# Kernel tuning notes

Measured on AMD Instinct MI355X. Metric: run time of the kernel, lower is better.

Reference implementation:

```python
import jax, jax.numpy as jnp
import numpy as np

N_NODES = 100000
F_IN, HID, OUT = 128, 64, 32


def setup_inputs() -> dict:
    key = jax.random.key(0)
    ks = jax.random.split(key, 16)
    x = jax.random.normal(ks[0], (N_NODES, F_IN), dtype=jnp.float32)
    edge_index = jax.random.randint(ks[1], (2, 3200000), 0, N_NODES, dtype=jnp.int64)
    edge_label_index = jax.random.randint(ks[2], (2, 1000000), 0, N_NODES, dtype=jnp.int64)
    def glorot(k, shape):
        lim = float(np.sqrt(6.0 / (shape[0] + shape[1])))
        return jax.random.uniform(k, shape, jnp.float32, -lim, lim)
    W1 = glorot(ks[3], (F_IN, HID)); b1 = jnp.zeros((HID,), jnp.float32)
    W2 = glorot(ks[4], (HID, HID)); b2 = jnp.zeros((HID,), jnp.float32)
    W3 = glorot(ks[5], (HID, OUT)); b3 = jnp.zeros((OUT,), jnp.float32)
    lpW1 = glorot(ks[6], (2 * OUT, HID)); lpb1 = jnp.zeros((HID,), jnp.float32)
    lpW2 = glorot(ks[7], (HID, 1)); lpb2 = jnp.zeros((1,), jnp.float32)
    return dict(x=x, edge_index=edge_index, edge_label_index=edge_label_index,
                W1=W1, b1=b1, W2=W2, b2=b2, W3=W3, b3=b3,
                lpW1=lpW1, lpb1=lpb1, lpW2=lpW2, lpb2=lpb2)


def _gcn_norm(edge_index, num_nodes):
    # PyG GCNConv default: add self-loops, symmetric normalization.
    self_loops = jnp.arange(num_nodes, dtype=edge_index.dtype)
    row = jnp.concatenate([edge_index[0], self_loops])  # source nodes
    col = jnp.concatenate([edge_index[1], self_loops])  # target nodes
    deg = jax.ops.segment_sum(jnp.ones_like(col, dtype=jnp.float32), col,
                              num_segments=num_nodes)
    dinv = jnp.where(deg > 0, jax.lax.rsqrt(deg), 0.0)
    norm = dinv[row] * dinv[col]  # [E + N]
    return row, col, norm


def _gcn_layer(x, W, b, row, col, norm, num_nodes):
    h = x @ W                               # [N, out]
    msg = h[row] * norm[:, None]            # gather + scale per edge
    agg = jax.ops.segment_sum(msg, col, num_segments=num_nodes)
    return agg + b


def reference(x, edge_index, edge_label_index, W1, b1, W2, b2, W3, b3,
              lpW1, lpb1, lpW2, lpb2):
    n = x.shape[0]
    row, col, norm = _gcn_norm(edge_index, n)
    # encode (eval mode: dropout is identity)
    z = jax.nn.relu(_gcn_layer(x, W1, b1, row, col, norm, n))
    z = jax.nn.relu(_gcn_layer(z, W2, b2, row, col, norm, n))
    z = _gcn_layer(z, W3, b3, row, col, norm, n)
    # decode: gather endpoint embeddings + MLP link predictor
    ef = jnp.concatenate([z[edge_label_index[0]], z[edge_label_index[1]]], axis=1)
    h = jax.nn.relu(ef @ lpW1 + lpb1)
    link_pred = h @ lpW2 + lpb2             # [E_label, 1]
    return link_pred, z
```

## Files before the change

### kernel.cpp

```cpp
#include <hip/hip_runtime.h>
#include <hip/hip_bf16.h>
#include <hip/hip_fp16.h>


#define BINA_CHUNK 8192


__global__ __launch_bounds__(512) void bhist_kernel(const int* __restrict__ colv,
                                                    int* __restrict__ chist,
                                                    int E, int nbuk) {
    __shared__ int hist[800];
    int base = blockIdx.x * BINA_CHUNK;
    int end = min(base + BINA_CHUNK, E);
    for (int i = threadIdx.x; i < nbuk; i += 512) hist[i] = 0;
    __syncthreads();
    int e = base + threadIdx.x * 4;
    for (; e + 4 <= end; e += 2048) {
        int4 c4 = *(const int4*)&colv[e];
        atomicAdd(&hist[c4.x >> 7], 1);
        atomicAdd(&hist[c4.y >> 7], 1);
        atomicAdd(&hist[c4.z >> 7], 1);
        atomicAdd(&hist[c4.w >> 7], 1);
    }
    for (; e < end; ++e) atomicAdd(&hist[colv[e] >> 7], 1);
    __syncthreads();
    for (int b = threadIdx.x; b < nbuk; b += 512)
        chist[(size_t)blockIdx.x * nbuk + b] = hist[b];
}


__global__ __launch_bounds__(256) void colscan_kernel(int* __restrict__ chist,
                                                      int* __restrict__ bcount,
                                                      int nchunk, int nbuk) {
    __shared__ int sh[256];
    const int b = blockIdx.x;
    const int c0 = threadIdx.x * 4;
    int v[4]; int s = 0;
#pragma unroll
    for (int i = 0; i < 4; ++i) {
        int c = c0 + i;
        v[i] = (c < nchunk) ? chist[(size_t)c * nbuk + b] : 0;
        s += v[i];
    }
    sh[threadIdx.x] = s;
    __syncthreads();
#pragma unroll
    for (int off = 1; off < 256; off <<= 1) {
        int y = (threadIdx.x >= (unsigned)off) ? sh[threadIdx.x - off] : 0;
        __syncthreads();
        sh[threadIdx.x] += y;
        __syncthreads();
    }
    int ex = sh[threadIdx.x] - s;
#pragma unroll
    for (int i = 0; i < 4; ++i) {
        int c = c0 + i;
        if (c < nchunk) { chist[(size_t)c * nbuk + b] = ex; ex += v[i]; }
    }
    if (threadIdx.x == 255) bcount[b] = sh[255];
}


__global__ __launch_bounds__(256) void bscan_kernel(const int* __restrict__ bcount,
                                                    int* __restrict__ bbase,
                                                    int nbuk, int* __restrict__ offsets, int N) {
    __shared__ int sh[256];
    int base = threadIdx.x * 4;
    int v[4]; int tsum = 0;
#pragma unroll
    for (int i = 0; i < 4; ++i) { int idx = base + i; v[i] = (idx < nbuk) ? bcount[idx] : 0; tsum += v[i]; }
    sh[threadIdx.x] = tsum;
    __syncthreads();
#pragma unroll
    for (int off = 1; off < 256; off <<= 1) {
        int y = (threadIdx.x >= (unsigned)off) ? sh[threadIdx.x - off] : 0;
        __syncthreads();
        sh[threadIdx.x] += y;
        __syncthreads();
    }
    int ex = sh[threadIdx.x] - tsum;
#pragma unroll
    for (int i = 0; i < 4; ++i) {
        int idx = base + i;
        if (idx < nbuk) { bbase[idx] = ex; ex += v[i]; }
        else if (idx == nbuk) { bbase[idx] = ex; offsets[N] = ex; }
    }
}


__global__ __launch_bounds__(512) void binA_kernel(const int* __restrict__ rowv,
                                                   const int* __restrict__ colv,
                                                   const int* __restrict__ chist,
                                                   const int* __restrict__ bbase,
                                                   int* __restrict__ pairs,
                                                   int E, int nbuk) {
    __shared__ int pos[800];
    int base = blockIdx.x * BINA_CHUNK;
    int end = min(base + BINA_CHUNK, E);
    for (int b = threadIdx.x; b < nbuk; b += 512)
        pos[b] = bbase[b] + chist[(size_t)blockIdx.x * nbuk + b];
    __syncthreads();
    int e = base + threadIdx.x * 4;
    for (; e + 4 <= end; e += 2048) {
        int4 c4 = *(const int4*)&colv[e];
        int4 r4 = *(const int4*)&rowv[e];
        int g0 = atomicAdd(&pos[c4.x >> 7], 1); pairs[g0] = (r4.x << 7) | (c4.x & 127);
        int g1 = atomicAdd(&pos[c4.y >> 7], 1); pairs[g1] = (r4.y << 7) | (c4.y & 127);
        int g2 = atomicAdd(&pos[c4.z >> 7], 1); pairs[g2] = (r4.z << 7) | (c4.z & 127);
        int g3 = atomicAdd(&pos[c4.w >> 7], 1); pairs[g3] = (r4.w << 7) | (c4.w & 127);
    }
    for (; e < end; ++e) {
        int c = colv[e];
        int g = atomicAdd(&pos[c >> 7], 1);
        pairs[g] = (rowv[e] << 7) | (c & 127);
    }
}


__global__ __launch_bounds__(512) void binB_kernel(const int* __restrict__ pairs,
                                                   const int* __restrict__ bbase,
                                                   int* __restrict__ offsets,
                                                   float* __restrict__ dinv,
                                                   int* __restrict__ edge_src, int N) {
    __shared__ int lcnt[128];
    __shared__ int sc[128];
    __shared__ int lcur[128];
    int nodeBeg = blockIdx.x << 7;
    int segBeg = bbase[blockIdx.x];
    int segEnd = bbase[blockIdx.x + 1];
    if (threadIdx.x < 128) lcnt[threadIdx.x] = 0;
    __syncthreads();
    for (int e = segBeg + threadIdx.x; e < segEnd; e += 512)
        atomicAdd(&lcnt[pairs[e] & 127], 1);
    __syncthreads();
    int v = (threadIdx.x < 128) ? lcnt[threadIdx.x] : 0;
    if (threadIdx.x < 128) sc[threadIdx.x] = v;
    __syncthreads();
    for (int off = 1; off < 128; off <<= 1) {
        int y = 0;
        if (threadIdx.x < 128 && threadIdx.x >= (unsigned)off) y = sc[threadIdx.x - off];
        __syncthreads();
        if (threadIdx.x < 128) sc[threadIdx.x] += y;
        __syncthreads();
    }
    if (threadIdx.x < 128) {
        int ex = sc[threadIdx.x] - v;
        lcur[threadIdx.x] = ex;
        int node = nodeBeg + threadIdx.x;
        if (node < N) {
            offsets[node] = segBeg + ex;
            dinv[node] = rsqrtf((float)(v + 1));
        }
    }
    __syncthreads();
    for (int e = segBeg + threadIdx.x; e < segEnd; e += 512) {
        int p = pairs[e];
        int rel = atomicAdd(&lcur[p & 127], 1);
        edge_src[segBeg + rel] = p >> 7;
    }
}


template <int K, int NOUT>
__global__ __launch_bounds__(32 * (NOUT / 4)) void gemm_scale(const float* __restrict__ in_,
                                                              const float* __restrict__ W,
                                                              const float* __restrict__ dinv,
                                                              __half* __restrict__ out, int N) {
    constexpr int TPB = 32 * (NOUT / 4);
    constexpr int KS = (K > 64) ? 64 : K;
    constexpr int XPITCH = KS + 4;
    __shared__ float xs[64 * XPITCH];
    __shared__ float ws[KS * NOUT];

    const int tid = threadIdx.x;
    const int nodeBase = blockIdx.x * 64;

    const int jg = tid % (NOUT / 4);
    const int ng = tid / (NOUT / 4);

    float acc[2][4];
#pragma unroll
    for (int i = 0; i < 2; ++i)
#pragma unroll
        for (int j = 0; j < 4; ++j) acc[i][j] = 0.f;

    for (int kh = 0; kh < K / KS; ++kh) {
        if (kh) __syncthreads();
        for (int i = tid; i < KS * NOUT / 4; i += TPB)
            *(float4*)&ws[i * 4] = *(const float4*)&W[(size_t)kh * KS * NOUT + i * 4];
        for (int i = tid; i < 64 * KS / 4; i += TPB) {
            int row = i / (KS / 4), c = i % (KS / 4);
            int src = nodeBase + row; if (src >= N) src = N - 1;
            *(float4*)&xs[row * XPITCH + c * 4] =
                *(const float4*)&in_[(size_t)src * K + kh * KS + c * 4];
        }
        __syncthreads();

#pragma unroll 4
        for (int kc = 0; kc < KS / 4; ++kc) {
            float4 xv[2], wv[4];
#pragma unroll
            for (int ni = 0; ni < 2; ++ni)
                xv[ni] = *(const float4*)&xs[(ng * 2 + ni) * XPITCH + kc * 4];
#pragma unroll
            for (int t = 0; t < 4; ++t)
                wv[t] = *(const float4*)&ws[(kc * 4 + t) * NOUT + jg * 4];
#pragma unroll
            for (int ni = 0; ni < 2; ++ni) {
                acc[ni][0] = fmaf(xv[ni].x, wv[0].x, acc[ni][0]);
                acc[ni][1] = fmaf(xv[ni].x, wv[0].y, acc[ni][1]);
                acc[ni][2] = fmaf(xv[ni].x, wv[0].z, acc[ni][2]);
                acc[ni][3] = fmaf(xv[ni].x, wv[0].w, acc[ni][3]);
                acc[ni][0] = fmaf(xv[ni].y, wv[1].x, acc[ni][0]);
                acc[ni][1] = fmaf(xv[ni].y, wv[1].y, acc[ni][1]);
                acc[ni][2] = fmaf(xv[ni].y, wv[1].z, acc[ni][2]);
                acc[ni][3] = fmaf(xv[ni].y, wv[1].w, acc[ni][3]);
                acc[ni][0] = fmaf(xv[ni].z, wv[2].x, acc[ni][0]);
                acc[ni][1] = fmaf(xv[ni].z, wv[2].y, acc[ni][1]);
                acc[ni][2] = fmaf(xv[ni].z, wv[2].z, acc[ni][2]);
                acc[ni][3] = fmaf(xv[ni].z, wv[2].w, acc[ni][3]);
                acc[ni][0] = fmaf(xv[ni].w, wv[3].x, acc[ni][0]);
                acc[ni][1] = fmaf(xv[ni].w, wv[3].y, acc[ni][1]);
                acc[ni][2] = fmaf(xv[ni].w, wv[3].z, acc[ni][2]);
                acc[ni][3] = fmaf(xv[ni].w, wv[3].w, acc[ni][3]);
            }
        }
    }

#pragma unroll
    for (int ni = 0; ni < 2; ++ni) {
        int node = nodeBase + ng * 2 + ni;
        if (node < N) {
            float dn = dinv[node];
            __half2* op = (__half2*)(out + (size_t)node * NOUT + jg * 4);
            op[0] = __floats2half2_rn(acc[ni][0] * dn, acc[ni][1] * dn);
            op[1] = __floats2half2_rn(acc[ni][2] * dn, acc[ni][3] * dn);
        }
    }
}


template <int F, bool RELU>
__global__ __launch_bounds__(256) void agg_pull(const __half* __restrict__ h,
                                                const float* __restrict__ dinv,
                                                const float* __restrict__ bias,
                                                const int* __restrict__ edge_src,
                                                const int* __restrict__ offsets,
                                                float* __restrict__ out, int N) {
    constexpr int LPN = F / 2;
    constexpr int GPW = 64 / LPN;
    int lane = threadIdx.x & 63;
    int wave = (blockIdx.x * 256 + (int)threadIdx.x) >> 6;
    int g = lane / LPN;
    int fl = lane % LPN;
    int node = wave * GPW + g;
    if (node >= N) return;
    float dn = dinv[node];
    int beg = offsets[node], end = offsets[node + 1];
    const __half2* __restrict__ hp = (const __half2*)h;

    float2 sv = __half22float2(hp[(size_t)node * LPN + fl]);
    float a0x = sv.x, a0y = sv.y;
    float a1x = 0.f, a1y = 0.f, a2x = 0.f, a2y = 0.f, a3x = 0.f, a3y = 0.f;

    int j = beg;
    for (; j + 8 <= end; j += 8) {
        int s0 = edge_src[j],     s1 = edge_src[j + 1], s2 = edge_src[j + 2], s3 = edge_src[j + 3];
        int s4 = edge_src[j + 4], s5 = edge_src[j + 5], s6 = edge_src[j + 6], s7 = edge_src[j + 7];
        __half2 v0 = hp[(size_t)s0 * LPN + fl];
        __half2 v1 = hp[(size_t)s1 * LPN + fl];
        __half2 v2 = hp[(size_t)s2 * LPN + fl];
        __half2 v3 = hp[(size_t)s3 * LPN + fl];
        __half2 v4 = hp[(size_t)s4 * LPN + fl];
        __half2 v5 = hp[(size_t)s5 * LPN + fl];
        __half2 v6 = hp[(size_t)s6 * LPN + fl];
        __half2 v7 = hp[(size_t)s7 * LPN + fl];
        float2 f0 = __half22float2(v0), f1 = __half22float2(v1);
        float2 f2 = __half22float2(v2), f3 = __half22float2(v3);
        float2 f4 = __half22float2(v4), f5 = __half22float2(v5);
        float2 f6 = __half22float2(v6), f7 = __half22float2(v7);
        a0x += f0.x; a0y += f0.y; a1x += f1.x; a1y += f1.y;
        a2x += f2.x; a2y += f2.y; a3x += f3.x; a3y += f3.y;
        a0x += f4.x; a0y += f4.y; a1x += f5.x; a1y += f5.y;
        a2x += f6.x; a2y += f6.y; a3x += f7.x; a3y += f7.y;
    }
    for (; j + 2 <= end; j += 2) {
        int s0 = edge_src[j], s1 = edge_src[j + 1];
        float2 f0 = __half22float2(hp[(size_t)s0 * LPN + fl]);
        float2 f1 = __half22float2(hp[(size_t)s1 * LPN + fl]);
        a0x += f0.x; a0y += f0.y; a1x += f1.x; a1y += f1.y;
    }
    if (j < end) {
        float2 f0 = __half22float2(hp[(size_t)edge_src[j] * LPN + fl]);
        a0x += f0.x; a0y += f0.y;
    }

    float2 bv = *(const float2*)&bias[fl * 2];
    float rx = ((a0x + a1x) + (a2x + a3x)) * dn + bv.x;
    float ry = ((a0y + a1y) + (a2y + a3y)) * dn + bv.y;
    if (RELU) { rx = fmaxf(rx, 0.f); ry = fmaxf(ry, 0.f); }
    *(float2*)&out[(size_t)node * F + fl * 2] = make_float2(rx, ry);
}


__global__ __launch_bounds__(512) void gemm_uv(const float* __restrict__ z,
                                               const float* __restrict__ W1,
                                               __half* __restrict__ uv, int N) {
    constexpr int ZPITCH = 36;
    __shared__ float zs[64 * ZPITCH];
    __shared__ float ws[64 * 64];
    const int tid = threadIdx.x;
    const int nodeBase = blockIdx.x * 64;

    for (int i = tid; i < 64 * 64 / 4; i += 512)
        *(float4*)&ws[i * 4] = *(const float4*)&W1[i * 4];
    for (int i = tid; i < 64 * 8; i += 512) {
        int row = i / 8, c = i % 8;
        int src = nodeBase + row; if (src >= N) src = N - 1;
        *(float4*)&zs[row * ZPITCH + c * 4] = *(const float4*)&z[(size_t)src * 32 + c * 4];
    }
    __syncthreads();

    const int jg = tid % 16;
    const int ng = tid / 16;

    float au[2][4], av[2][4];
#pragma unroll
    for (int i = 0; i < 2; ++i)
#pragma unroll
        for (int j = 0; j < 4; ++j) { au[i][j] = 0.f; av[i][j] = 0.f; }

#pragma unroll 4
    for (int kc = 0; kc < 8; ++kc) {
        float4 xv[2], wu[4], wv2[4];
#pragma unroll
        for (int ni = 0; ni < 2; ++ni)
            xv[ni] = *(const float4*)&zs[(ng * 2 + ni) * ZPITCH + kc * 4];
#pragma unroll
        for (int t = 0; t < 4; ++t) {
            wu[t]  = *(const float4*)&ws[(kc * 4 + t) * 64 + jg * 4];
            wv2[t] = *(const float4*)&ws[(32 + kc * 4 + t) * 64 + jg * 4];
        }
#pragma unroll
        for (int ni = 0; ni < 2; ++ni) {
            float xk[4] = {xv[ni].x, xv[ni].y, xv[ni].z, xv[ni].w};
#pragma unroll
            for (int t = 0; t < 4; ++t) {
                au[ni][0] = fmaf(xk[t], wu[t].x, au[ni][0]);
                au[ni][1] = fmaf(xk[t], wu[t].y, au[ni][1]);
                au[ni][2] = fmaf(xk[t], wu[t].z, au[ni][2]);
                au[ni][3] = fmaf(xk[t], wu[t].w, au[ni][3]);
                av[ni][0] = fmaf(xk[t], wv2[t].x, av[ni][0]);
                av[ni][1] = fmaf(xk[t], wv2[t].y, av[ni][1]);
                av[ni][2] = fmaf(xk[t], wv2[t].z, av[ni][2]);
                av[ni][3] = fmaf(xk[t], wv2[t].w, av[ni][3]);
            }
        }
    }

#pragma unroll
    for (int ni = 0; ni < 2; ++ni) {
        int node = nodeBase + ng * 2 + ni;
        if (node < N) {
            __half2* pu = (__half2*)(uv + (size_t)node * 128 + jg * 4);
            pu[0] = __floats2half2_rn(au[ni][0], au[ni][1]);
            pu[1] = __floats2half2_rn(au[ni][2], au[ni][3]);
            __half2* pv = (__half2*)(uv + (size_t)node * 128 + 64 + jg * 4);
            pv[0] = __floats2half2_rn(av[ni][0], av[ni][1]);
            pv[1] = __floats2half2_rn(av[ni][2], av[ni][3]);
        }
    }
}


__global__ __launch_bounds__(256) void decode_edge(const __half* __restrict__ uv,
                                                   const int* __restrict__ eli, int EL,
                                                   const float* __restrict__ lpb1,
                                                   const float* __restrict__ lpW2,
                                                   const float* __restrict__ lpb2,
                                                   float* __restrict__ out) {
    const int sub = threadIdx.x & 7;
    float4 b1a = *(const float4*)&lpb1[sub * 8];
    float4 b1b = *(const float4*)&lpb1[sub * 8 + 4];
    float4 w2a = *(const float4*)&lpW2[sub * 8];
    float4 w2b = *(const float4*)&lpW2[sub * 8 + 4];
    const float b2v = lpb2[0];
    int e = blockIdx.x * 32 + (threadIdx.x >> 3);
    if (e >= EL) return;
    int a = eli[e], b = eli[EL + e];
    float4 ra = *(const float4*)(uv + (size_t)a * 128 + sub * 8);
    float4 rb = *(const float4*)(uv + (size_t)b * 128 + 64 + sub * 8);
    float2 a01 = __half22float2(*(const __half2*)&ra.x);
    float2 a23 = __half22float2(*(const __half2*)&ra.y);
    float2 a45 = __half22float2(*(const __half2*)&ra.z);
    float2 a67 = __half22float2(*(const __half2*)&ra.w);
    float2 b01 = __half22float2(*(const __half2*)&rb.x);
    float2 b23 = __half22float2(*(const __half2*)&rb.y);
    float2 b45 = __half22float2(*(const __half2*)&rb.z);
    float2 b67 = __half22float2(*(const __half2*)&rb.w);
    float p = fmaxf(a01.x + b01.x + b1a.x, 0.f) * w2a.x;
    p = fmaf(fmaxf(a01.y + b01.y + b1a.y, 0.f), w2a.y, p);
    p = fmaf(fmaxf(a23.x + b23.x + b1a.z, 0.f), w2a.z, p);
    p = fmaf(fmaxf(a23.y + b23.y + b1a.w, 0.f), w2a.w, p);
    p = fmaf(fmaxf(a45.x + b45.x + b1b.x, 0.f), w2b.x, p);
    p = fmaf(fmaxf(a45.y + b45.y + b1b.y, 0.f), w2b.y, p);
    p = fmaf(fmaxf(a67.x + b67.x + b1b.z, 0.f), w2b.z, p);
    p = fmaf(fmaxf(a67.y + b67.y + b1b.w, 0.f), w2b.w, p);
    p += __shfl_down(p, 4, 8);
    p += __shfl_down(p, 2, 8);
    p += __shfl_down(p, 1, 8);
    if (sub == 0) out[e] = p + b2v;
}


extern "C" void kernel_launch(void* const* d_in, const int* in_sizes, int n_in,
                              void* d_out, int out_size, void* d_ws, size_t ws_size,
                              hipStream_t stream) {
    const float* x    = (const float*)d_in[0];
    const int* ei     = (const int*)d_in[1];
    const int* eli    = (const int*)d_in[2];
    const float* W1   = (const float*)d_in[3];
    const float* b1   = (const float*)d_in[4];
    const float* W2   = (const float*)d_in[5];
    const float* b2   = (const float*)d_in[6];
    const float* W3   = (const float*)d_in[7];
    const float* b3   = (const float*)d_in[8];
    const float* lpW1 = (const float*)d_in[9];
    const float* lpb1 = (const float*)d_in[10];
    const float* lpW2 = (const float*)d_in[11];
    const float* lpb2 = (const float*)d_in[12];

    const int N  = in_sizes[0] / 128;
    const int E  = in_sizes[1] / 2;
    const int EL = in_sizes[2] / 2;

    char* p = (char*)d_ws;
    auto alloc = [&](size_t bytes) { void* r = (void*)p; p += (bytes + 255) & ~(size_t)255; return r; };
    float* dinv     = (float*)alloc((size_t)N * 4);
    int*   offsets  = (int*)alloc((size_t)(N + 1) * 4);
    int*   bcount   = (int*)alloc(1024 * 4);
    int*   bbase    = (int*)alloc(1024 * 4);
    int*   edge_src = (int*)alloc((size_t)E * 4);
    __half* bufG    = (__half*)alloc((size_t)N * 64 * 2);
    float* bufZ     = (float*)alloc((size_t)N * 64 * 4);
    __half* uvbuf   = (__half*)alloc((size_t)N * 128 * 2);
    int*   pairs    = (int*)uvbuf;
    int*   chist    = (int*)bufZ;

    const int* rowv = ei;
    const int* colv = ei + E;

    int nbuk = (N + 127) / 128;
    int nchunk = (E + BINA_CHUNK - 1) / BINA_CHUNK;

    bhist_kernel<<<nchunk, 512, 0, stream>>>(colv, chist, E, nbuk);
    colscan_kernel<<<nbuk, 256, 0, stream>>>(chist, bcount, nchunk, nbuk);
    bscan_kernel<<<1, 256, 0, stream>>>(bcount, bbase, nbuk, offsets, N);
    binA_kernel<<<nchunk, 512, 0, stream>>>(rowv, colv, chist, bbase, pairs, E, nbuk);
    binB_kernel<<<nbuk, 512, 0, stream>>>(pairs, bbase, offsets, dinv, edge_src, N);

    float* zout = (float*)d_out + EL;

    int gblocks = (N + 63) / 64;

    int aggblocks64 = (N + 7) / 8;
    int aggblocks32 = (N + 15) / 16;

    gemm_scale<128, 64><<<gblocks, 512, 0, stream>>>(x, W1, dinv, bufG, N);
    agg_pull<64, true><<<aggblocks64, 256, 0, stream>>>(bufG, dinv, b1, edge_src, offsets, bufZ, N);
    gemm_scale<64, 64><<<gblocks, 512, 0, stream>>>(bufZ, W2, dinv, bufG, N);
    agg_pull<64, true><<<aggblocks64, 256, 0, stream>>>(bufG, dinv, b2, edge_src, offsets, bufZ, N);
    gemm_scale<64, 32><<<gblocks, 256, 0, stream>>>(bufZ, W3, dinv, bufG, N);
    agg_pull<32, false><<<aggblocks32, 256, 0, stream>>>(bufG, dinv, b3, edge_src, offsets, zout, N);
    gemm_uv<<<gblocks, 512, 0, stream>>>(zout, lpW1, uvbuf, N);
    decode_edge<<<(EL + 31) / 32, 256, 0, stream>>>(uvbuf, eli, EL, lpb1, lpW2, lpb2, (float*)d_out);
}
```

Baseline: 462.9 us.

## Use 16-byte half8 gathers per lane and shuffle-broadcast edge indices in pull aggregation

The pull aggregation kernel now gives each lane 8 half features, loaded as one 16-byte float4, instead of 2 features. That cuts lanes per node by 4x, so each wave handles 4x more nodes. Edge source indices are loaded cooperatively, one per lane, and broadcast with wave shuffles instead of each lane reloading them. The launch grid shrinks to match. In exchange, there is less memory-level parallelism per node and more load imbalance across lanes within a wave, since each lane group now covers several nodes with different degrees.

```diff
diff --git a/kernel.cpp b/kernel.cpp
--- a/kernel.cpp
+++ b/kernel.cpp
@@ -247,59 +247,83 @@
                                                 const int* __restrict__ edge_src,
                                                 const int* __restrict__ offsets,
                                                 float* __restrict__ out, int N) {
-    constexpr int LPN = F / 2;
+    constexpr int LPN = F / 8;
     constexpr int GPW = 64 / LPN;
+    constexpr int UNR = LPN;
     int lane = threadIdx.x & 63;
     int wave = (blockIdx.x * 256 + (int)threadIdx.x) >> 6;
     int g = lane / LPN;
     int fl = lane % LPN;
+    int gbase = lane & ~(LPN - 1);
     int node = wave * GPW + g;
     if (node >= N) return;
     float dn = dinv[node];
     int beg = offsets[node], end = offsets[node + 1];
-    const __half2* __restrict__ hp = (const __half2*)h;
-
-    float2 sv = __half22float2(hp[(size_t)node * LPN + fl]);
-    float a0x = sv.x, a0y = sv.y;
-    float a1x = 0.f, a1y = 0.f, a2x = 0.f, a2y = 0.f, a3x = 0.f, a3y = 0.f;
+    const float4* __restrict__ hp4 = (const float4*)h;
+
+    float4 sv = hp4[(size_t)node * LPN + fl];
+    float2 s0 = __half22float2(*(const __half2*)&sv.x);
+    float2 s1 = __half22float2(*(const __half2*)&sv.y);
+    float2 s2 = __half22float2(*(const __half2*)&sv.z);
+    float2 s3 = __half22float2(*(const __half2*)&sv.w);
+    float aA[8] = {s0.x, s0.y, s1.x, s1.y, s2.x, s2.y, s3.x, s3.y};
+    float aB[8] = {0.f, 0.f, 0.f, 0.f, 0.f, 0.f, 0.f, 0.f};
 
     int j = beg;
-    for (; j + 8 <= end; j += 8) {
-        int s0 = edge_src[j],     s1 = edge_src[j + 1], s2 = edge_src[j + 2], s3 = edge_src[j + 3];
-        int s4 = edge_src[j + 4], s5 = edge_src[j + 5], s6 = edge_src[j + 6], s7 = edge_src[j + 7];
-        __half2 v0 = hp[(size_t)s0 * LPN + fl];
-        __half2 v1 = hp[(size_t)s1 * LPN + fl];
-        __half2 v2 = hp[(size_t)s2 * LPN + fl];
-        __half2 v3 = hp[(size_t)s3 * LPN + fl];
-        __half2 v4 = hp[(size_t)s4 * LPN + fl];
-        __half2 v5 = hp[(size_t)s5 * LPN + fl];
-        __half2 v6 = hp[(size_t)s6 * LPN + fl];
-        __half2 v7 = hp[(size_t)s7 * LPN + fl];
-        float2 f0 = __half22float2(v0), f1 = __half22float2(v1);
-        float2 f2 = __half22float2(v2), f3 = __half22float2(v3);
-        float2 f4 = __half22float2(v4), f5 = __half22float2(v5);
-        float2 f6 = __half22float2(v6), f7 = __half22float2(v7);
-        a0x += f0.x; a0y += f0.y; a1x += f1.x; a1y += f1.y;
-        a2x += f2.x; a2y += f2.y; a3x += f3.x; a3y += f3.y;
-        a0x += f4.x; a0y += f4.y; a1x += f5.x; a1y += f5.y;
-        a2x += f6.x; a2y += f6.y; a3x += f7.x; a3y += f7.y;
-    }
-    for (; j + 2 <= end; j += 2) {
-        int s0 = edge_src[j], s1 = edge_src[j + 1];
-        float2 f0 = __half22float2(hp[(size_t)s0 * LPN + fl]);
-        float2 f1 = __half22float2(hp[(size_t)s1 * LPN + fl]);
-        a0x += f0.x; a0y += f0.y; a1x += f1.x; a1y += f1.y;
+    for (; j + UNR <= end; j += UNR) {
+        int smy = edge_src[j + fl];
+        int sk[UNR];
+#pragma unroll
+        for (int k = 0; k < UNR; ++k)
+            sk[k] = __shfl(smy, gbase + k, 64);
+        float4 v[UNR];
+#pragma unroll
+        for (int k = 0; k < UNR; ++k)
+            v[k] = hp4[(size_t)sk[k] * LPN + fl];
+#pragma unroll
+        for (int k = 0; k < UNR; ++k) {
+            float2 p0 = __half22float2(*(const __half2*)&v[k].x);
+            float2 p1 = __half22float2(*(const __half2*)&v[k].y);
+            float2 p2 = __half22float2(*(const __half2*)&v[k].z);
+            float2 p3 = __half22float2(*(const __half2*)&v[k].w);
+            float* a = (k & 1) ? aB : aA;
+            a[0] += p0.x; a[1] += p0.y; a[2] += p1.x; a[3] += p1.y;
+            a[4] += p2.x; a[5] += p2.y; a[6] += p3.x; a[7] += p3.y;
+        }
     }
     if (j < end) {
-        float2 f0 = __half22float2(hp[(size_t)edge_src[j] * LPN + fl]);
-        a0x += f0.x; a0y += f0.y;
-    }
-
-    float2 bv = *(const float2*)&bias[fl * 2];
-    float rx = ((a0x + a1x) + (a2x + a3x)) * dn + bv.x;
-    float ry = ((a0y + a1y) + (a2y + a3y)) * dn + bv.y;
-    if (RELU) { rx = fmaxf(rx, 0.f); ry = fmaxf(ry, 0.f); }
-    *(float2*)&out[(size_t)node * F + fl * 2] = make_float2(rx, ry);
+        int r = end - j;
+        int smy = (fl < r) ? edge_src[j + fl] : 0;
+        for (int k = 0; k < r; ++k) {
+            int sk = __shfl(smy, gbase + k, 64);
+            float4 v = hp4[(size_t)sk * LPN + fl];
+            float2 p0 = __half22float2(*(const __half2*)&v.x);
+            float2 p1 = __half22float2(*(const __half2*)&v.y);
+            float2 p2 = __half22float2(*(const __half2*)&v.z);
+            float2 p3 = __half22float2(*(const __half2*)&v.w);
+            float* a = (k & 1) ? aB : aA;
+            a[0] += p0.x; a[1] += p0.y; a[2] += p1.x; a[3] += p1.y;
+            a[4] += p2.x; a[5] += p2.y; a[6] += p3.x; a[7] += p3.y;
+        }
+    }
+
+    float4 bva = *(const float4*)&bias[fl * 8];
+    float4 bvb = *(const float4*)&bias[fl * 8 + 4];
+    float r0 = (aA[0] + aB[0]) * dn + bva.x;
+    float r1 = (aA[1] + aB[1]) * dn + bva.y;
+    float r2 = (aA[2] + aB[2]) * dn + bva.z;
+    float r3 = (aA[3] + aB[3]) * dn + bva.w;
+    float r4 = (aA[4] + aB[4]) * dn + bvb.x;
+    float r5 = (aA[5] + aB[5]) * dn + bvb.y;
+    float r6 = (aA[6] + aB[6]) * dn + bvb.z;
+    float r7 = (aA[7] + aB[7]) * dn + bvb.w;
+    if (RELU) {
+        r0 = fmaxf(r0, 0.f); r1 = fmaxf(r1, 0.f); r2 = fmaxf(r2, 0.f); r3 = fmaxf(r3, 0.f);
+        r4 = fmaxf(r4, 0.f); r5 = fmaxf(r5, 0.f); r6 = fmaxf(r6, 0.f); r7 = fmaxf(r7, 0.f);
+    }
+    float* op = &out[(size_t)node * F + fl * 8];
+    *(float4*)op = make_float4(r0, r1, r2, r3);
+    *(float4*)(op + 4) = make_float4(r4, r5, r6, r7);
 }
 
 
@@ -463,8 +487,8 @@
 
     int gblocks = (N + 63) / 64;
 
-    int aggblocks64 = (N + 7) / 8;
-    int aggblocks32 = (N + 15) / 16;
+    int aggblocks64 = (N + 31) / 32;
+    int aggblocks32 = (N + 63) / 64;
 
     gemm_scale<128, 64><<<gblocks, 512, 0, stream>>>(x, W1, dinv, bufG, N);
     agg_pull<64, true><<<aggblocks64, 256, 0, stream>>>(bufG, dinv, b1, edge_src, offsets, bufZ, N);
```

After: 457.8 us. No clear change (-1.1%).
